# Kernel optimization log

Hardware: AMD Instinct MI355X
Metric: run time of the kernel (lower is better)

Reference implementation:

```python
import jax, jax.numpy as jnp
import numpy as np

DIM = 192
HEADS = 6
HD = DIM // HEADS            # 32
RES = (32, 64, 64)           # D, H, W
WS = (4, 4, 4)               # window size
NW_TOK = WS[0] * WS[1] * WS[2]   # 64 tokens per window
L = RES[0] * RES[1] * RES[2]     # 131072
HIDDEN = 4 * DIM
B = 2


def _rel_pos_index():
    # faithful to the torch buffer construction (3D branch)
    coords = np.stack(np.meshgrid(*[np.arange(w) for w in WS], indexing='ij'))  # (3, wd, wh, ww)
    cf = coords.reshape(3, -1)                     # (3, 64)
    rel = cf[:, :, None] - cf[:, None, :]          # (3, 64, 64)
    rel = rel.transpose(1, 2, 0).astype(np.int64)  # (64, 64, 3)
    for i in range(3):
        rel[:, :, i] += WS[i] - 1
    rel[:, :, 0] *= (2 * WS[1] - 1) * (2 * WS[2] - 1)
    rel[:, :, 1] *= 2 * WS[2] - 1
    return rel.sum(-1)                             # (64, 64)


def setup_inputs() -> dict:
    key = jax.random.key(0)
    ks = jax.random.split(key, 8)
    s = 0.02
    d = {}
    d['skip'] = jax.random.normal(ks[0], (B, L, DIM), jnp.float32)
    d['x_up'] = jax.random.normal(ks[1], (B, L, DIM), jnp.float32)
    # norms
    d['g1'] = jnp.ones((DIM,), jnp.float32); d['be1'] = jnp.zeros((DIM,), jnp.float32)
    d['g2'] = jnp.ones((DIM,), jnp.float32); d['be2'] = jnp.zeros((DIM,), jnp.float32)
    # attention params
    d['Wkv'] = jax.random.normal(ks[2], (DIM, 2 * DIM), jnp.float32) * s
    d['bkv'] = jnp.zeros((2 * DIM,), jnp.float32)
    d['Wproj'] = jax.random.normal(ks[3], (DIM, DIM), jnp.float32) * s
    d['bproj'] = jnp.zeros((DIM,), jnp.float32)
    d['bias_table'] = jax.random.normal(ks[4], ((2 * WS[0] - 1) * (2 * WS[1] - 1) * (2 * WS[2] - 1), HEADS), jnp.float32) * s
    d['rel_idx'] = jnp.asarray(_rel_pos_index(), jnp.int32)
    # MLP params
    d['W1'] = jax.random.normal(ks[5], (DIM, HIDDEN), jnp.float32) * s
    d['b1'] = jnp.zeros((HIDDEN,), jnp.float32)
    d['W2'] = jax.random.normal(ks[6], (HIDDEN, DIM), jnp.float32) * s
    d['b2'] = jnp.zeros((DIM,), jnp.float32)
    return d


def _ln(x, g, b):
    mu = x.mean(-1, keepdims=True)
    var = x.var(-1, keepdims=True)
    return (x - mu) * jax.lax.rsqrt(var + 1e-5) * g + b


def _win_part(x):
    # x: (B, D, H, W, C) -> (B*nW, 64, C)
    D, H, W = RES; wd, wh, ww = WS
    x = x.reshape(B, D // wd, wd, H // wh, wh, W // ww, ww, DIM)
    x = x.transpose(0, 1, 3, 5, 2, 4, 6, 7)
    return x.reshape(-1, NW_TOK, DIM)


def _win_rev(w):
    # (B*nW, 64, C) -> (B, L, C)
    D, H, W = RES; wd, wh, ww = WS
    x = w.reshape(B, D // wd, H // wh, W // ww, wd, wh, ww, DIM)
    x = x.transpose(0, 1, 4, 2, 5, 3, 6, 7)
    return x.reshape(B, L, DIM)


def reference(skip, x_up, g1, be1, g2, be2, Wkv, bkv, Wproj, bproj,
              bias_table, rel_idx, W1, b1, W2, b2):
    shortcut = skip
    s = _ln(skip, g1, be1).reshape(B, *RES, DIM)
    u = _ln(x_up, g1, be1).reshape(B, *RES, DIM)
    sw = _win_part(s)   # kv source: (Bw, 64, C)
    uw = _win_part(u)   # q source
    Bw = sw.shape[0]
    kv = (sw @ Wkv + bkv).reshape(Bw, NW_TOK, 2, HEADS, HD)
    k = kv[:, :, 0].transpose(0, 2, 1, 3)   # (Bw, h, 64, hd)
    v = kv[:, :, 1].transpose(0, 2, 1, 3)
    q = uw.reshape(Bw, NW_TOK, HEADS, HD).transpose(0, 2, 1, 3)
    scale = HD ** -0.5
    attn = jnp.einsum('bhqd,bhkd->bhqk', q * scale, k)
    bias = bias_table[rel_idx.reshape(-1)].reshape(NW_TOK, NW_TOK, HEADS).transpose(2, 0, 1)
    attn = jax.nn.softmax(attn + bias[None], axis=-1)
    o = jnp.einsum('bhqk,bhkd->bhqd', attn, v).transpose(0, 2, 1, 3).reshape(Bw, NW_TOK, DIM)
    o = o @ Wproj + bproj
    x = shortcut + _win_rev(o)
    h = _ln(x, g2, be2)
    h = jax.nn.gelu(h @ W1 + b1, approximate=False)
    return x + (h @ W2 + b2)
```

## Files before the change

### kernel.cpp

```cpp
#include <hip/hip_runtime.h>
#include <hip/hip_bf16.h>

typedef __hip_bfloat16 bf16;
typedef short s8v __attribute__((ext_vector_type(8)));
typedef float f32x4 __attribute__((ext_vector_type(4)));

__device__ __forceinline__ float b2f(bf16 v) { return __bfloat162float(v); }
__device__ __forceinline__ bf16 f2b(float v) { return __float2bfloat16(v); }

union H8 { bf16 h[8]; s8v v; uint2 u2[2]; };
union H4 { bf16 h[4]; unsigned int u[2]; };
union U4V { unsigned int u[4]; s8v v; };

__device__ __forceinline__ float gelu_f(float x) {
    float x2 = x * x;
    float t = fmaf(x2, 0.044715f, 1.0f);
    float u = x * 1.5957691216057308f * t;
    float e = __expf(-u);
    return x / (1.0f + e);
}

__device__ __forceinline__ void stage_frag(const bf16* __restrict__ img, bf16* lds,
                                           int nseg, int wv, int lane) {
    for (int seg = wv; seg < nseg; seg += 4) {
        __builtin_amdgcn_global_load_lds(
            (const __attribute__((address_space(1))) void*)(img + seg * 512 + (lane << 3)),
            (__attribute__((address_space(3))) void*)(lds + seg * 512),
            16, 0, 0);
    }
}

__global__ __launch_bounds__(256) void k_prep(
    const float* __restrict__ Wkv, const float* __restrict__ Wproj,
    const float* __restrict__ W1,  const float* __restrict__ W2,
    bf16* __restrict__ ws)
{
    int t = blockIdx.x * 256 + threadIdx.x;
    if (t >= 50688) return;
    int k, n, ld;
    const float* W;
    bf16* dst;
    if (t < 9216) {
        int c = t / 1152, r = t % 1152;
        int tile = r >> 6, lane = r & 63;
        int ks = tile / 3, nt = tile % 3;
        n = c * 48 + nt * 16 + (lane & 15);
        k = ks * 32 + (lane >> 4) * 8;
        W = Wkv; ld = 384; dst = ws + t * 8;
    } else if (t < 13824) {
        int t2 = t - 9216;
        int c = t2 / 1152, r = t2 % 1152;
        int tile = r >> 6, lane = r & 63;
        int ks = tile / 3, nt = tile % 3;
        n = c * 48 + nt * 16 + (lane & 15);
        k = ks * 32 + (lane >> 4) * 8;
        W = Wproj; ld = 192; dst = ws + 73728 + t2 * 8;
    } else {
        int t3 = t - 13824;
        int c = t3 / 1536, r = t3 % 1536;
        int half = r / 768, rr = r % 768;
        int tile = rr >> 6, lane = rr & 63;
        int lr = lane & 15, g = lane >> 4;
        if (half == 0) {
            int ks = tile >> 1, nt2 = tile & 1;
            n = c * 32 + nt2 * 16 + lr; k = ks * 32 + g * 8; W = W1; ld = 768;
        } else {
            n = tile * 16 + lr; k = c * 32 + g * 8; W = W2; ld = 192;
        }
        dst = ws + 110592 + t3 * 8;
    }
    #pragma unroll
    for (int e = 0; e < 8; ++e) dst[e] = f2b(W[(k + e) * ld + n]);
}

__global__ __launch_bounds__(256, 2) void k_attn(
    const float* __restrict__ skip, const float* __restrict__ xup,
    const float* __restrict__ g1,   const float* __restrict__ be1,
    const bf16*  __restrict__ imgKv,const float* __restrict__ bkv,
    const bf16*  __restrict__ imgPr,const float* __restrict__ bproj,
    const float* __restrict__ btab, const int*  __restrict__ relidx,
    float* __restrict__ xout)
{
    __shared__ __align__(16) bf16 sK[64 * 200];
    __shared__ __align__(16) char poolRaw[36864];
    __shared__ __align__(16) float sBt[2058];

    bf16* sVt = (bf16*)poolRaw;
    bf16* sP  = (bf16*)(poolRaw + 27648);
    bf16* sO  = (bf16*)poolRaw;

    const int tid = threadIdx.x;
    const int lane = tid & 63;
    const int wv = tid >> 6;
    const int g = lane >> 4;
    const int lr = lane & 15;
    const int w = blockIdx.x;
    const int b = w >> 11;
    const int widx = w & 2047;
    const int d0 = widx >> 8, h0 = (widx >> 4) & 15, w0 = widx & 15;

    #define GROW(t) (b * 131072 + (d0 * 4 + ((t) >> 4)) * 4096 + \
                     (h0 * 4 + (((t) >> 2) & 3)) * 64 + (w0 * 4 + ((t) & 3)))

    const int myrow = wv * 16 + lr;
    const int growA = GROW(myrow) * 192;
    float4 u4[12], s4[12];
    #pragma unroll
    for (int ks = 0; ks < 6; ++ks) {
        int k0 = 32 * ks + 8 * g;
        u4[2 * ks]     = *(const float4*)(xup  + growA + k0);
        u4[2 * ks + 1] = *(const float4*)(xup  + growA + k0 + 4);
        s4[2 * ks]     = *(const float4*)(skip + growA + k0);
        s4[2 * ks + 1] = *(const float4*)(skip + growA + k0 + 4);
    }
    float su = 0, squ = 0, ss = 0, sqs = 0;
    #pragma unroll
    for (int i = 0; i < 12; ++i) {
        const float* up = &u4[i].x;
        const float* sp = &s4[i].x;
        #pragma unroll
        for (int e = 0; e < 4; ++e) {
            su += up[e]; squ += up[e] * up[e];
            ss += sp[e]; sqs += sp[e] * sp[e];
        }
    }
    su += __shfl_xor(su, 16);  su += __shfl_xor(su, 32);
    squ += __shfl_xor(squ, 16); squ += __shfl_xor(squ, 32);
    ss += __shfl_xor(ss, 16);  ss += __shfl_xor(ss, 32);
    sqs += __shfl_xor(sqs, 16); sqs += __shfl_xor(sqs, 32);
    const float inv192 = 1.f / 192.f;
    float muU = su * inv192, vU = squ * inv192 - muU * muU;
    float muS = ss * inv192, vS = sqs * inv192 - muS * muS;
    float rU = rsqrtf(vU + 1e-5f), rS = rsqrtf(vS + 1e-5f);
    const float scale = 0.17677669529663687f;

    s8v qreg[6], sreg[6];
    #pragma unroll
    for (int ks = 0; ks < 6; ++ks) {
        H8 qa, sa;
        #pragma unroll
        for (int half = 0; half < 2; ++half) {
            const float* up = &u4[2 * ks + half].x;
            const float* sp = &s4[2 * ks + half].x;
            #pragma unroll
            for (int e = 0; e < 4; ++e) {
                int k = 32 * ks + 8 * g + 4 * half + e;
                float gg = g1[k], bb = be1[k];
                qa.h[4 * half + e] = f2b(((up[e] - muU) * rU * gg + bb) * scale);
                sa.h[4 * half + e] = f2b((sp[e] - muS) * rS * gg + bb);
            }
        }
        qreg[ks] = qa.v; sreg[ks] = sa.v;
    }

    for (int i = tid; i < 2058; i += 256) sBt[i] = btab[i];

    for (int nc = 0; nc < 8; ++nc) {
        const bf16* img = imgKv + nc * 9216;
        f32x4 acc[3];
        #pragma unroll
        for (int nt = 0; nt < 3; ++nt) acc[nt] = (f32x4){0.f, 0.f, 0.f, 0.f};
        #pragma unroll
        for (int ks = 0; ks < 6; ++ks) {
            #pragma unroll
            for (int nt = 0; nt < 3; ++nt) {
                s8v bfr = *(const s8v*)(img + ((ks * 3 + nt) * 64 + lane) * 8);
                acc[nt] = __builtin_amdgcn_mfma_f32_16x16x32_bf16(sreg[ks], bfr, acc[nt], 0, 0, 0);
            }
        }
        if (nc < 4) {
            #pragma unroll
            for (int nt = 0; nt < 3; ++nt) {
                int c = nc * 48 + nt * 16 + lr;
                float bias = bkv[c];
                #pragma unroll
                for (int e = 0; e < 4; ++e)
                    sK[(wv * 16 + 4 * g + e) * 200 + c] = f2b(acc[nt][e] + bias);
            }
        } else {
            #pragma unroll
            for (int nt = 0; nt < 3; ++nt) {
                int c = nc * 48 + nt * 16 + lr;
                float bias = bkv[c];
                int d = c - 192;
                H8 t4;
                #pragma unroll
                for (int e = 0; e < 4; ++e) t4.h[e] = f2b(acc[nt][e] + bias);
                *(uint2*)(sVt + d * 72 + wv * 16 + 4 * g) = t4.u2[0];
            }
        }
    }

    int bidx[4][4];
    #pragma unroll
    for (int nt = 0; nt < 4; ++nt)
        #pragma unroll
        for (int e = 0; e < 4; ++e)
            bidx[nt][e] = relidx[(wv * 16 + lr) * 64 + nt * 16 + 4 * g + e] * 6;

    __syncthreads();

    f32x4 accOT[6][2];
    #pragma unroll
    for (int h = 0; h < 6; ++h)
        #pragma unroll
        for (int nt = 0; nt < 2; ++nt) accOT[h][nt] = (f32x4){0.f, 0.f, 0.f, 0.f};

    #pragma unroll
    for (int h = 0; h < 6; ++h) {
        f32x4 s[4];
        #pragma unroll
        for (int nt = 0; nt < 4; ++nt) {
            s8v kf = *(const s8v*)(sK + (nt * 16 + lr) * 200 + h * 32 + 8 * g);
            s[nt] = __builtin_amdgcn_mfma_f32_16x16x32_bf16(kf, qreg[h],
                        (f32x4){0.f, 0.f, 0.f, 0.f}, 0, 0, 0);
        }
        #pragma unroll
        for (int nt = 0; nt < 4; ++nt)
            #pragma unroll
            for (int e = 0; e < 4; ++e)
                s[nt][e] += sBt[bidx[nt][e] + h];
        float mx = -1e30f;
        #pragma unroll
        for (int nt = 0; nt < 4; ++nt)
            #pragma unroll
            for (int e = 0; e < 4; ++e) mx = fmaxf(mx, s[nt][e]);
        mx = fmaxf(mx, __shfl_xor(mx, 16));
        mx = fmaxf(mx, __shfl_xor(mx, 32));
        float sm = 0;
        #pragma unroll
        for (int nt = 0; nt < 4; ++nt)
            #pragma unroll
            for (int e = 0; e < 4; ++e) { s[nt][e] = __expf(s[nt][e] - mx); sm += s[nt][e]; }
        sm += __shfl_xor(sm, 16);
        sm += __shfl_xor(sm, 32);
        float iv = 1.f / sm;
        #pragma unroll
        for (int nt = 0; nt < 4; ++nt) {
            H8 pk;
            #pragma unroll
            for (int e = 0; e < 4; ++e) pk.h[e] = f2b(s[nt][e] * iv);
            *(uint2*)(sP + (wv * 16 + lr) * 72 + nt * 16 + 4 * g) = pk.u2[0];
        }
        s8v aP0 = *(const s8v*)(sP + (wv * 16 + lr) * 72 + 8 * g);
        s8v aP1 = *(const s8v*)(sP + (wv * 16 + lr) * 72 + 32 + 8 * g);
        #pragma unroll
        for (int nt = 0; nt < 2; ++nt) {
            const bf16* vb = sVt + (h * 32 + nt * 16 + lr) * 72;
            s8v v0 = *(const s8v*)(vb + 8 * g);
            s8v v1 = *(const s8v*)(vb + 32 + 8 * g);
            accOT[h][nt] = __builtin_amdgcn_mfma_f32_16x16x32_bf16(v0, aP0, accOT[h][nt], 0, 0, 0);
            accOT[h][nt] = __builtin_amdgcn_mfma_f32_16x16x32_bf16(v1, aP1, accOT[h][nt], 0, 0, 0);
        }
    }

    __syncthreads();

    #pragma unroll
    for (int h = 0; h < 6; ++h)
        #pragma unroll
        for (int nt = 0; nt < 2; ++nt) {
            H8 pk;
            #pragma unroll
            for (int e = 0; e < 4; ++e) pk.h[e] = f2b(accOT[h][nt][e]);
            *(uint2*)(sO + (wv * 16 + lr) * 200 + h * 32 + nt * 16 + 4 * g) = pk.u2[0];
        }
    s8v aO[6];
    #pragma unroll
    for (int ks = 0; ks < 6; ++ks)
        aO[ks] = *(const s8v*)(sO + (wv * 16 + lr) * 200 + 32 * ks + 8 * g);

    int gq[4];
    #pragma unroll
    for (int e = 0; e < 4; ++e) gq[e] = GROW(wv * 16 + 4 * g + e) * 192;

    for (int nc = 0; nc < 4; ++nc) {
        const bf16* img = imgPr + nc * 9216;
        f32x4 acc[3];
        #pragma unroll
        for (int nt = 0; nt < 3; ++nt) acc[nt] = (f32x4){0.f, 0.f, 0.f, 0.f};
        #pragma unroll
        for (int ks = 0; ks < 6; ++ks) {
            #pragma unroll
            for (int nt = 0; nt < 3; ++nt) {
                s8v bfr = *(const s8v*)(img + ((ks * 3 + nt) * 64 + lane) * 8);
                acc[nt] = __builtin_amdgcn_mfma_f32_16x16x32_bf16(aO[ks], bfr, acc[nt], 0, 0, 0);
            }
        }
        #pragma unroll
        for (int nt = 0; nt < 3; ++nt) {
            int c = nc * 48 + nt * 16 + lr;
            float bp = bproj[c];
            #pragma unroll
            for (int e = 0; e < 4; ++e) {
                int go = gq[e] + c;
                xout[go] = acc[nt][e] + bp + skip[go];
            }
        }
    }
    #undef GROW
}

__global__ __launch_bounds__(256, 3) void k_mlp(
    float* __restrict__ xio,
    const float* __restrict__ g2, const float* __restrict__ be2,
    const bf16*  __restrict__ imgMlp,
    const float* __restrict__ b1, const float* __restrict__ b2)
{
    __shared__ __align__(1024) bf16 sW[2][12288];

    const int tid = threadIdx.x;
    const int lane = tid & 63;
    const int wv = tid >> 6;
    const int g = lane >> 4;
    const int lr = lane & 15;
    const int rowbase = blockIdx.x * 64;

    stage_frag(imgMlp,         sW[0], 24, wv, lane);
    stage_frag(imgMlp + 12288, sW[1], 24, wv, lane);

    s8v xreg[6];
    {
        const int row = rowbase + wv * 16 + lr;
        float4 xa[12];
        #pragma unroll
        for (int ks = 0; ks < 6; ++ks) {
            int k0 = 32 * ks + 8 * g;
            xa[2 * ks]     = *(const float4*)(xio + row * 192 + k0);
            xa[2 * ks + 1] = *(const float4*)(xio + row * 192 + k0 + 4);
        }
        float s = 0, sq = 0;
        #pragma unroll
        for (int i = 0; i < 12; ++i) {
            const float* p = &xa[i].x;
            #pragma unroll
            for (int e = 0; e < 4; ++e) { s += p[e]; sq += p[e] * p[e]; }
        }
        s += __shfl_xor(s, 16);  s += __shfl_xor(s, 32);
        sq += __shfl_xor(sq, 16); sq += __shfl_xor(sq, 32);
        float mu = s * (1.f / 192.f), var = sq * (1.f / 192.f) - mu * mu;
        float rs = rsqrtf(var + 1e-5f);
        #pragma unroll
        for (int ks = 0; ks < 6; ++ks) {
            H8 xa8;
            #pragma unroll
            for (int half = 0; half < 2; ++half) {
                int k0 = 32 * ks + 8 * g + 4 * half;
                float4 gg = *(const float4*)(g2 + k0);
                float4 be = *(const float4*)(be2 + k0);
                const float* p = &xa[2 * ks + half].x;
                const float* gp = &gg.x;
                const float* bp = &be.x;
                #pragma unroll
                for (int e = 0; e < 4; ++e)
                    xa8.h[4 * half + e] = f2b((p[e] - mu) * rs * gp[e] + bp[e]);
            }
            xreg[ks] = xa8.v;
        }
    }

    f32x4 accC[12];
    #pragma unroll
    for (int nt = 0; nt < 12; ++nt) accC[nt] = (f32x4){0.f, 0.f, 0.f, 0.f};

    const int s0lane = ((g & 1) * 2) * 16 + lr;
    const int s1lane = s0lane + 16;
    const bool hiHalf = (g >= 2);

    for (int ch = 0; ch < 24; ++ch) {
        if (ch < 23) asm volatile("s_waitcnt vmcnt(6)" ::: "memory");
        else         asm volatile("s_waitcnt vmcnt(0)" ::: "memory");
        __builtin_amdgcn_sched_barrier(0);
        __builtin_amdgcn_s_barrier();
        __builtin_amdgcn_sched_barrier(0);
        const bf16* wc = sW[ch & 1];

        f32x4 accHT[2];
        accHT[0] = (f32x4){0.f, 0.f, 0.f, 0.f};
        accHT[1] = (f32x4){0.f, 0.f, 0.f, 0.f};
        #pragma unroll
        for (int ks = 0; ks < 6; ++ks) {
            s8v w0 = *(const s8v*)(wc + ((ks * 2 + 0) * 64 + lane) * 8);
            s8v w1 = *(const s8v*)(wc + ((ks * 2 + 1) * 64 + lane) * 8);
            accHT[0] = __builtin_amdgcn_mfma_f32_16x16x32_bf16(w0, xreg[ks], accHT[0], 0, 0, 0);
            accHT[1] = __builtin_amdgcn_mfma_f32_16x16x32_bf16(w1, xreg[ks], accHT[1], 0, 0, 0);
        }

        s8v aH;
        {
            unsigned int pk[2][2];
            #pragma unroll
            for (int nt2 = 0; nt2 < 2; ++nt2) {
                float4 b1v = *(const float4*)(b1 + ch * 32 + nt2 * 16 + 4 * g);
                const float* bp = &b1v.x;
                H4 t;
                #pragma unroll
                for (int e = 0; e < 4; ++e)
                    t.h[e] = f2b(gelu_f(accHT[nt2][e] + bp[e]));
                pk[nt2][0] = t.u[0];
                pk[nt2][1] = t.u[1];
            }
            U4V o;
            int a00 = __shfl((int)pk[0][0], s0lane), a10 = __shfl((int)pk[1][0], s0lane);
            int a01 = __shfl((int)pk[0][1], s0lane), a11 = __shfl((int)pk[1][1], s0lane);
            int b00 = __shfl((int)pk[0][0], s1lane), b10 = __shfl((int)pk[1][0], s1lane);
            int b01 = __shfl((int)pk[0][1], s1lane), b11 = __shfl((int)pk[1][1], s1lane);
            o.u[0] = (unsigned int)(hiHalf ? a10 : a00);
            o.u[1] = (unsigned int)(hiHalf ? a11 : a01);
            o.u[2] = (unsigned int)(hiHalf ? b10 : b00);
            o.u[3] = (unsigned int)(hiHalf ? b11 : b01);
            aH = o.v;
        }

        #pragma unroll
        for (int nt = 0; nt < 12; ++nt) {
            s8v bW = *(const s8v*)(wc + 6144 + (nt * 64 + lane) * 8);
            accC[nt] = __builtin_amdgcn_mfma_f32_16x16x32_bf16(aH, bW, accC[nt], 0, 0, 0);
        }

        __builtin_amdgcn_sched_barrier(0);
        __builtin_amdgcn_s_barrier();
        __builtin_amdgcn_sched_barrier(0);
        if (ch < 22)
            stage_frag(imgMlp + (ch + 2) * 12288, sW[ch & 1], 24, wv, lane);
    }

    #pragma unroll
    for (int nt = 0; nt < 12; ++nt) {
        int col = nt * 16 + lr;
        float bb = b2[col];
        #pragma unroll
        for (int e = 0; e < 4; ++e) {
            int row = rowbase + wv * 16 + g * 4 + e;
            float* p = xio + row * 192 + col;
            *p = accC[nt][e] + bb + *p;
        }
    }
}

extern "C" void kernel_launch(void* const* d_in, const int* in_sizes, int n_in,
                              void* d_out, int out_size, void* d_ws, size_t ws_size,
                              hipStream_t stream) {
    const float* skip   = (const float*)d_in[0];
    const float* xup    = (const float*)d_in[1];
    const float* g1     = (const float*)d_in[2];
    const float* be1    = (const float*)d_in[3];
    const float* g2     = (const float*)d_in[4];
    const float* be2    = (const float*)d_in[5];
    const float* Wkv    = (const float*)d_in[6];
    const float* bkv    = (const float*)d_in[7];
    const float* Wproj  = (const float*)d_in[8];
    const float* bproj  = (const float*)d_in[9];
    const float* btab   = (const float*)d_in[10];
    const int*  relidx  = (const int*)d_in[11];
    const float* W1     = (const float*)d_in[12];
    const float* b1     = (const float*)d_in[13];
    const float* W2     = (const float*)d_in[14];
    const float* b2     = (const float*)d_in[15];
    float* xio = (float*)d_out;
    bf16* ws = (bf16*)d_ws;

    k_prep<<<198, 256, 0, stream>>>(Wkv, Wproj, W1, W2, ws);
    k_attn<<<4096, 256, 0, stream>>>(skip, xup, g1, be1, ws, bkv,
                                     ws + 73728, bproj, btab, relidx, xio);
    k_mlp<<<4096, 256, 0, stream>>>(xio, g2, be2, ws + 110592, b1, b2);
}
```

Baseline: 584.4 us.

## Fuse attention and MLP into one kernel keeping residual in registers

Merges the windowed attention kernel and the MLP kernel into a single kernel per window. The post-attention residual stays in registers, and LayerNorm2 is computed via cross-lane shuffles then staged through LDS. This removes the fp32 intermediate write and reread through global memory. In exchange the MLP weight staging loses its double-buffered async prefetch: each chunk is loaded and then waited on with two full barriers, and register pressure rises under the tighter 2-block occupancy bound.

```diff
diff --git a/kernel.cpp b/kernel.cpp
--- a/kernel.cpp
+++ b/kernel.cpp
@@ -73,13 +73,16 @@
     for (int e = 0; e < 8; ++e) dst[e] = f2b(W[(k + e) * ld + n]);
 }
 
-__global__ __launch_bounds__(256, 2) void k_attn(
+__global__ __launch_bounds__(256, 2) void k_fused(
     const float* __restrict__ skip, const float* __restrict__ xup,
     const float* __restrict__ g1,   const float* __restrict__ be1,
     const bf16*  __restrict__ imgKv,const float* __restrict__ bkv,
     const bf16*  __restrict__ imgPr,const float* __restrict__ bproj,
     const float* __restrict__ btab, const int*  __restrict__ relidx,
-    float* __restrict__ xout)
+    const float* __restrict__ g2,   const float* __restrict__ be2,
+    const bf16*  __restrict__ imgMlp,
+    const float* __restrict__ b1,   const float* __restrict__ b2,
+    float* __restrict__ out)
 {
     __shared__ __align__(16) bf16 sK[64 * 200];
     __shared__ __align__(16) char poolRaw[36864];
@@ -88,6 +91,8 @@
     bf16* sVt = (bf16*)poolRaw;
     bf16* sP  = (bf16*)(poolRaw + 27648);
     bf16* sO  = (bf16*)poolRaw;
+    bf16* sX  = sK;
+    bf16* sW  = (bf16*)poolRaw;
 
     const int tid = threadIdx.x;
     const int lane = tid & 63;
@@ -274,6 +279,7 @@
     #pragma unroll
     for (int e = 0; e < 4; ++e) gq[e] = GROW(wv * 16 + 4 * g + e) * 192;
 
+    float xf[12][4];
     for (int nc = 0; nc < 4; ++nc) {
         const bf16* img = imgPr + nc * 9216;
         f32x4 acc[3];
@@ -288,76 +294,40 @@
             }
         }
         #pragma unroll
-        for (int nt = 0; nt < 3; ++nt) {
-            int c = nc * 48 + nt * 16 + lr;
+        for (int nt3 = 0; nt3 < 3; ++nt3) {
+            int c = nc * 48 + nt3 * 16 + lr;
             float bp = bproj[c];
             #pragma unroll
-            for (int e = 0; e < 4; ++e) {
-                int go = gq[e] + c;
-                xout[go] = acc[nt][e] + bp + skip[go];
-            }
-        }
-    }
-    #undef GROW
-}
-
-__global__ __launch_bounds__(256, 3) void k_mlp(
-    float* __restrict__ xio,
-    const float* __restrict__ g2, const float* __restrict__ be2,
-    const bf16*  __restrict__ imgMlp,
-    const float* __restrict__ b1, const float* __restrict__ b2)
-{
-    __shared__ __align__(1024) bf16 sW[2][12288];
-
-    const int tid = threadIdx.x;
-    const int lane = tid & 63;
-    const int wv = tid >> 6;
-    const int g = lane >> 4;
-    const int lr = lane & 15;
-    const int rowbase = blockIdx.x * 64;
-
-    stage_frag(imgMlp,         sW[0], 24, wv, lane);
-    stage_frag(imgMlp + 12288, sW[1], 24, wv, lane);
-
-    s8v xreg[6];
-    {
-        const int row = rowbase + wv * 16 + lr;
-        float4 xa[12];
-        #pragma unroll
-        for (int ks = 0; ks < 6; ++ks) {
-            int k0 = 32 * ks + 8 * g;
-            xa[2 * ks]     = *(const float4*)(xio + row * 192 + k0);
-            xa[2 * ks + 1] = *(const float4*)(xio + row * 192 + k0 + 4);
-        }
+            for (int e = 0; e < 4; ++e)
+                xf[nc * 3 + nt3][e] = acc[nt3][e] + bp + skip[gq[e] + c];
+        }
+    }
+
+    #pragma unroll
+    for (int e = 0; e < 4; ++e) {
         float s = 0, sq = 0;
         #pragma unroll
-        for (int i = 0; i < 12; ++i) {
-            const float* p = &xa[i].x;
-            #pragma unroll
-            for (int e = 0; e < 4; ++e) { s += p[e]; sq += p[e] * p[e]; }
-        }
-        s += __shfl_xor(s, 16);  s += __shfl_xor(s, 32);
-        sq += __shfl_xor(sq, 16); sq += __shfl_xor(sq, 32);
+        for (int j = 0; j < 12; ++j) { s += xf[j][e]; sq += xf[j][e] * xf[j][e]; }
+        s += __shfl_xor(s, 1); s += __shfl_xor(s, 2);
+        s += __shfl_xor(s, 4); s += __shfl_xor(s, 8);
+        sq += __shfl_xor(sq, 1); sq += __shfl_xor(sq, 2);
+        sq += __shfl_xor(sq, 4); sq += __shfl_xor(sq, 8);
         float mu = s * (1.f / 192.f), var = sq * (1.f / 192.f) - mu * mu;
         float rs = rsqrtf(var + 1e-5f);
-        #pragma unroll
-        for (int ks = 0; ks < 6; ++ks) {
-            H8 xa8;
-            #pragma unroll
-            for (int half = 0; half < 2; ++half) {
-                int k0 = 32 * ks + 8 * g + 4 * half;
-                float4 gg = *(const float4*)(g2 + k0);
-                float4 be = *(const float4*)(be2 + k0);
-                const float* p = &xa[2 * ks + half].x;
-                const float* gp = &gg.x;
-                const float* bp = &be.x;
-                #pragma unroll
-                for (int e = 0; e < 4; ++e)
-                    xa8.h[4 * half + e] = f2b((p[e] - mu) * rs * gp[e] + bp[e]);
-            }
-            xreg[ks] = xa8.v;
-        }
-    }
+        int row = wv * 16 + 4 * g + e;
+        #pragma unroll
+        for (int j = 0; j < 12; ++j) {
+            int c = j * 16 + lr;
+            sX[row * 200 + c] = f2b((xf[j][e] - mu) * rs * g2[c] + be2[c]);
+        }
+    }
+
+    __syncthreads();
+
+    s8v xreg[6];
+    #pragma unroll
+    for (int ks = 0; ks < 6; ++ks)
+        xreg[ks] = *(const s8v*)(sX + (wv * 16 + lr) * 200 + 32 * ks + 8 * g);
 
     f32x4 accC[12];
     #pragma unroll
@@ -368,20 +338,16 @@
     const bool hiHalf = (g >= 2);
 
     for (int ch = 0; ch < 24; ++ch) {
-        if (ch < 23) asm volatile("s_waitcnt vmcnt(6)" ::: "memory");
-        else         asm volatile("s_waitcnt vmcnt(0)" ::: "memory");
-        __builtin_amdgcn_sched_barrier(0);
-        __builtin_amdgcn_s_barrier();
-        __builtin_amdgcn_sched_barrier(0);
-        const bf16* wc = sW[ch & 1];
+        stage_frag(imgMlp + ch * 12288, sW, 24, wv, lane);
+        __syncthreads();
 
         f32x4 accHT[2];
         accHT[0] = (f32x4){0.f, 0.f, 0.f, 0.f};
         accHT[1] = (f32x4){0.f, 0.f, 0.f, 0.f};
         #pragma unroll
         for (int ks = 0; ks < 6; ++ks) {
-            s8v w0 = *(const s8v*)(wc + ((ks * 2 + 0) * 64 + lane) * 8);
-            s8v w1 = *(const s8v*)(wc + ((ks * 2 + 1) * 64 + lane) * 8);
+            s8v w0 = *(const s8v*)(sW + ((ks * 2 + 0) * 64 + lane) * 8);
+            s8v w1 = *(const s8v*)(sW + ((ks * 2 + 1) * 64 + lane) * 8);
             accHT[0] = __builtin_amdgcn_mfma_f32_16x16x32_bf16(w0, xreg[ks], accHT[0], 0, 0, 0);
             accHT[1] = __builtin_amdgcn_mfma_f32_16x16x32_bf16(w1, xreg[ks], accHT[1], 0, 0, 0);
         }
@@ -414,28 +380,21 @@
 
         #pragma unroll
         for (int nt = 0; nt < 12; ++nt) {
-            s8v bW = *(const s8v*)(wc + 6144 + (nt * 64 + lane) * 8);
+            s8v bW = *(const s8v*)(sW + 6144 + (nt * 64 + lane) * 8);
             accC[nt] = __builtin_amdgcn_mfma_f32_16x16x32_bf16(aH, bW, accC[nt], 0, 0, 0);
         }
-
-        __builtin_amdgcn_sched_barrier(0);
-        __builtin_amdgcn_s_barrier();
-        __builtin_amdgcn_sched_barrier(0);
-        if (ch < 22)
-            stage_frag(imgMlp + (ch + 2) * 12288, sW[ch & 1], 24, wv, lane);
+        __syncthreads();
     }
 
     #pragma unroll
     for (int nt = 0; nt < 12; ++nt) {
-        int col = nt * 16 + lr;
-        float bb = b2[col];
-        #pragma unroll
-        for (int e = 0; e < 4; ++e) {
-            int row = rowbase + wv * 16 + g * 4 + e;
-            float* p = xio + row * 192 + col;
-            *p = accC[nt][e] + bb + *p;
-        }
-    }
+        int c = nt * 16 + lr;
+        float bb = b2[c];
+        #pragma unroll
+        for (int e = 0; e < 4; ++e)
+            out[gq[e] + c] = xf[nt][e] + accC[nt][e] + bb;
+    }
+    #undef GROW
 }
 
 extern "C" void kernel_launch(void* const* d_in, const int* in_sizes, int n_in,
@@ -457,11 +416,11 @@
     const float* b1     = (const float*)d_in[13];
     const float* W2     = (const float*)d_in[14];
     const float* b2     = (const float*)d_in[15];
-    float* xio = (float*)d_out;
     bf16* ws = (bf16*)d_ws;
 
     k_prep<<<198, 256, 0, stream>>>(Wkv, Wproj, W1, W2, ws);
-    k_attn<<<4096, 256, 0, stream>>>(skip, xup, g1, be1, ws, bkv,
-                                     ws + 73728, bproj, btab, relidx, xio);
-    k_mlp<<<4096, 256, 0, stream>>>(xio, g2, be2, ws + 110592, b1, b2);
+    k_fused<<<4096, 256, 0, stream>>>(skip, xup, g1, be1, ws, bkv,
+                                      ws + 73728, bproj, btab, relidx,
+                                      g2, be2, ws + 110592, b1, b2,
+                                      (float*)d_out);
 }
```

After: 564.4 us. 3.4% less time.
